# Performance work log

Measured on AMD Instinct MI355X. Metric: run time of the kernel, lower is better.

## Reference

```python
import jax, jax.numpy as jnp
import numpy as np

B, S = 128, 128
AH, VH, TH = 64, 64, 128  # audio/vision/text LSTM hidden sizes
FUSED = (AH + 1) * (VH + 1) * (TH + 1)  # 545025
PF = 128  # post_fusion_dim


def setup_inputs() -> dict:
    key = jax.random.key(0)
    ks = jax.random.split(key, 6)
    return {
        "audio_h": jax.random.normal(ks[0], (B, S, AH), jnp.float32),
        "vision_h": jax.random.normal(ks[1], (B, S, VH), jnp.float32),
        "text_h": jax.random.normal(ks[2], (B, S, TH), jnp.float32),
        "W1": jax.random.normal(ks[3], (PF, FUSED), jnp.float32) * 0.001,
        "b1": jnp.zeros((PF,), jnp.float32),
        "W2": jax.random.normal(ks[4], (PF, PF), jnp.float32) * 0.05,
        "b2": jnp.zeros((PF,), jnp.float32),
        "W3": jax.random.normal(ks[5], (1, PF), jnp.float32) * 0.05,
        "b3": jnp.zeros((1,), jnp.float32),
    }


def reference(audio_h, vision_h, text_h, W1, b1, W2, b2, W3, b3):
    b, s = audio_h.shape[0], audio_h.shape[1]
    ones = jnp.ones((b, s, 1), audio_h.dtype)
    a = jnp.concatenate([ones, audio_h], axis=2)   # [B,S,AH+1]
    v = jnp.concatenate([ones, vision_h], axis=2)  # [B,S,VH+1]
    t = jnp.concatenate([ones, text_h], axis=2)    # [B,S,TH+1]
    # sum_t outer(a_t, v_t, t_t): one fused contraction over the time axis
    fusion = jnp.einsum('bsa,bsv,bsw->bavw', a, v, t)  # [B,AH+1,VH+1,TH+1]
    fusion = fusion.reshape(b, -1)                      # matches torch view order (a,v,t)
    # T2FN low-rank regularizer scale
    tmp = jnp.sqrt(jnp.asarray(AH * VH * TH / max(AH, VH, TH), jnp.float32))
    # post-fusion MLP (dropout p=0 -> identity)
    y1 = jax.nn.relu(fusion @ W1.T + b1)
    y2 = jax.nn.relu(y1 @ W2.T + b2)
    out = y2 @ W3.T + b3  # [B,1]
    out = jax.nn.sigmoid(out) * 6.0 - 3.0  # output_range=6, output_shift=-3
    norm = jnp.linalg.norm(fusion, axis=1)  # [B]
    reg_loss = jnp.mean(tmp * norm)
    return (out, reg_loss)
```

## Files before the change

### kernel.cpp

```cpp
#include <hip/hip_runtime.h>
#include <math.h>

#define BB 128
#define SS 128
#define AE 65
#define VE 65
#define TE 129
#define PFD 128
#define FUSED 545025UL
#define FUSEDI 545025
#define VSTRIDE 136
#define APLANE 8840
#define FPP 574976UL
#define FPPI 574976
#define KSP 512
#define NBLK 1123

typedef _Float16 half8 __attribute__((ext_vector_type(8)));
typedef float f32x16 __attribute__((ext_vector_type(16)));

__device__ __forceinline__ void gll4(const void* g, void* l) {
  __builtin_amdgcn_global_load_lds((const __attribute__((address_space(1))) void*)g,
                                   (__attribute__((address_space(3))) void*)l, 4, 0, 0);
}
__device__ __forceinline__ void gll16(const void* g, void* l) {
  __builtin_amdgcn_global_load_lds((const __attribute__((address_space(1))) void*)g,
                                   (__attribute__((address_space(3))) void*)l, 16, 0, 0);
}

__global__ __launch_bounds__(256) void k_zero(float* __restrict__ p, int n) {
  int i = blockIdx.x * 256 + threadIdx.x;
  if (i < n) p[i] = 0.f;
}

__global__ __launch_bounds__(256) void k_fpad(_Float16* __restrict__ Fh) {
  const int b = blockIdx.x;
  _Float16* base = Fh + (size_t)b * FPP;
  for (int i = threadIdx.x; i < 29575; i += 256) {
    const int a = i / 455, r = i - a * 455;
    const int v = r / 7, e = r - v * 7;
    base[a * APLANE + v * VSTRIDE + 129 + e] = (_Float16)0.f;
  }
  for (int i = threadIdx.x; i < 376; i += 256) base[574600 + i] = (_Float16)0.f;
}

__global__ __launch_bounds__(256) void k_core(
    const float* __restrict__ audio, const float* __restrict__ vision,
    const float* __restrict__ text, _Float16* __restrict__ Fh,
    float* __restrict__ normsq)
{
  const int b  = blockIdx.x;
  const int gy = blockIdx.y;
  const int gz = blockIdx.z;
  const int tid = threadIdx.x;
  const int wv = tid >> 6, ln = tid & 63;
  const int lr = ln & 31, hb = ln >> 5;

  __shared__ float    sVt[64][132];
  __shared__ float    sAc[8][132];
  __shared__ _Float16 sTh[64][136];
  __shared__ _Float16 sTl[64][136];

  {
    const float* vb = vision + (size_t)b * SS * 64;
#pragma unroll
    for (int r = 0; r < 32; ++r) {
      const int e = tid + 256 * r;
      sVt[e & 63][e >> 6] = vb[e];
    }
    const float* ab = audio + (size_t)b * SS * 64 + 8 * gy;
#pragma unroll
    for (int r = 0; r < 4; ++r) {
      const int e = tid + 256 * r;
      sAc[e & 7][e >> 3] = ab[(e >> 3) * 64 + (e & 7)];
    }
    const int wbase = 64 * gz;
    const float* tb = text + (size_t)b * SS * 128;
#pragma unroll
    for (int r = 0; r < 32; ++r) {
      const int e = tid + 256 * r;
      const int s = e >> 6, wl = e & 63;
      const int w = wbase + wl;
      const float val = (w == 0) ? 1.f : tb[s * 128 + w - 1];
      const _Float16 th = (_Float16)val;
      sTh[wl][s] = th;
      sTl[wl][s] = (_Float16)((val - (float)th) * 2048.f);
    }
  }
  __syncthreads();

  float ss = 0.f;
  for (int i = 0; i < 8; ++i) {
    const int u  = 8 * wv + i;
    const int rt = u >> 1, wt = u & 1;
    const int j  = rt >> 1, vh = rt & 1;
    const int v0m = 32 * vh;
    const int wl0 = 32 * wt;

    f32x16 acc = {}, accl = {};
#pragma unroll
    for (int ks = 0; ks < 8; ++ks) {
      const int s0 = 16 * ks + 8 * hb;
      const float4 x0 = *(const float4*)&sVt[v0m + lr][s0];
      const float4 x1 = *(const float4*)&sVt[v0m + lr][s0 + 4];
      const float4 a0 = *(const float4*)&sAc[j][s0];
      const float4 a1 = *(const float4*)&sAc[j][s0 + 4];
      const float pp[8] = {a0.x * x0.x, a0.y * x0.y, a0.z * x0.z, a0.w * x0.w,
                           a1.x * x1.x, a1.y * x1.y, a1.z * x1.z, a1.w * x1.w};
      half8 afh, afl;
#pragma unroll
      for (int e = 0; e < 8; ++e) {
        const _Float16 h = (_Float16)pp[e];
        afh[e] = h;
        afl[e] = (_Float16)((pp[e] - (float)h) * 2048.f);
      }
      const half8 bqh = *(const half8*)&sTh[wl0 + lr][s0];
      const half8 bql = *(const half8*)&sTl[wl0 + lr][s0];
      acc  = __builtin_amdgcn_mfma_f32_32x32x16_f16(afh, bqh, acc,  0, 0, 0);
      accl = __builtin_amdgcn_mfma_f32_32x32x16_f16(afl, bqh, accl, 0, 0, 0);
      accl = __builtin_amdgcn_mfma_f32_32x32x16_f16(afh, bql, accl, 0, 0, 0);
    }

    const int a = 1 + 8 * gy + j;
    _Float16* Fb = Fh + (size_t)b * FPP + (size_t)a * APLANE;
    const int wg = 64 * gz + wl0 + lr;
#pragma unroll
    for (int reg = 0; reg < 16; ++reg) {
      const int crow = (reg & 3) + 8 * (reg >> 2) + 4 * hb;
      const int v = 1 + 32 * vh + crow;
      const float f = acc[reg] + accl[reg] * (1.f / 2048.f);
      ss += f * f;
      Fb[(size_t)v * VSTRIDE + wg] = (_Float16)f;
    }
  }

#pragma unroll
  for (int off = 32; off > 0; off >>= 1) ss += __shfl_down(ss, off);
  if (ln == 0) atomicAdd(&normsq[b], ss);
}

__global__ __launch_bounds__(256) void k_pa(
    const float* __restrict__ vision, const float* __restrict__ text,
    _Float16* __restrict__ Fh, float* __restrict__ normsq)
{
  const int b = blockIdx.x;
  const int tid = threadIdx.x;
  const int tw = tid & 15, tv = tid >> 4;
  __shared__ float sv[32][80];
  __shared__ float st[32][144];
  float acc[5][9];
#pragma unroll
  for (int i = 0; i < 5; ++i)
#pragma unroll
    for (int j = 0; j < 9; ++j) acc[i][j] = 0.f;

  for (int c = 0; c < 4; ++c) {
    const int s0 = 32 * c;
    __syncthreads();
    const float* vbase = &vision[((size_t)(b * SS + s0)) * 64];
#pragma unroll
    for (int r = 0; r < 8; ++r) {
      const int e = tid + 256 * r;
      sv[e >> 6][(e & 63) + 1] = vbase[e];
    }
    const float* tbase = &text[((size_t)(b * SS + s0)) * 128];
#pragma unroll
    for (int r = 0; r < 16; ++r) {
      const int e = tid + 256 * r;
      st[e >> 7][(e & 127) + 1] = tbase[e];
    }
    if (tid < 32) { sv[tid][0] = 1.f; st[tid][0] = 1.f; }
    __syncthreads();
    for (int s = 0; s < 32; ++s) {
      float vr[5], tr[9];
#pragma unroll
      for (int i = 0; i < 5; ++i) {
        const int vx = tv + 16 * i;
        vr[i] = (vx < VE) ? sv[s][vx] : 0.f;
      }
#pragma unroll
      for (int j = 0; j < 9; ++j) {
        const int wx = tw + 16 * j;
        tr[j] = (wx < TE) ? st[s][wx] : 0.f;
      }
#pragma unroll
      for (int i = 0; i < 5; ++i)
#pragma unroll
        for (int j = 0; j < 9; ++j) acc[i][j] += vr[i] * tr[j];
    }
  }
  _Float16* Fb = Fh + (size_t)b * FPP;
  float ss = 0.f;
#pragma unroll
  for (int i = 0; i < 5; ++i) {
    const int v = tv + 16 * i;
    if (v < VE) {
#pragma unroll
      for (int j = 0; j < 9; ++j) {
        const int w = tw + 16 * j;
        if (w < TE) {
          const float m = acc[i][j];
          Fb[(size_t)v * VSTRIDE + w] = (_Float16)m;
          ss += m * m;
        }
      }
    }
  }
#pragma unroll
  for (int off = 32; off > 0; off >>= 1) ss += __shfl_down(ss, off);
  if ((tid & 63) == 0) atomicAdd(&normsq[b], ss);
}

__global__ __launch_bounds__(256) void k_pv(
    const float* __restrict__ audio, const float* __restrict__ text,
    _Float16* __restrict__ Fh, float* __restrict__ normsq)
{
  const int b = blockIdx.x;
  const int tid = threadIdx.x;
  const int tw = tid & 15, tv = tid >> 4;
  __shared__ float sa[32][64];
  __shared__ float st[32][144];
  float acc[4][9];
#pragma unroll
  for (int i = 0; i < 4; ++i)
#pragma unroll
    for (int j = 0; j < 9; ++j) acc[i][j] = 0.f;

  for (int c = 0; c < 4; ++c) {
    const int s0 = 32 * c;
    __syncthreads();
    const float* abase = &audio[((size_t)(b * SS + s0)) * 64];
#pragma unroll
    for (int r = 0; r < 8; ++r) {
      const int e = tid + 256 * r;
      sa[e >> 6][e & 63] = abase[e];
    }
    const float* tbase = &text[((size_t)(b * SS + s0)) * 128];
#pragma unroll
    for (int r = 0; r < 16; ++r) {
      const int e = tid + 256 * r;
      st[e >> 7][(e & 127) + 1] = tbase[e];
    }
    if (tid < 32) st[tid][0] = 1.f;
    __syncthreads();
    for (int s = 0; s < 32; ++s) {
      float ar[4], tr[9];
#pragma unroll
      for (int i = 0; i < 4; ++i) ar[i] = sa[s][tv + 16 * i];
#pragma unroll
      for (int j = 0; j < 9; ++j) {
        const int wx = tw + 16 * j;
        tr[j] = (wx < TE) ? st[s][wx] : 0.f;
      }
#pragma unroll
      for (int i = 0; i < 4; ++i)
#pragma unroll
        for (int j = 0; j < 9; ++j) acc[i][j] += ar[i] * tr[j];
    }
  }
  float ss = 0.f;
#pragma unroll
  for (int i = 0; i < 4; ++i) {
    const int a = 1 + tv + 16 * i;
    _Float16* Fb = Fh + (size_t)b * FPP + (size_t)a * APLANE;
#pragma unroll
    for (int j = 0; j < 9; ++j) {
      const int w = tw + 16 * j;
      if (w < TE) {
        const float m = acc[i][j];
        Fb[w] = (_Float16)m;
        ss += m * m;
      }
    }
  }
#pragma unroll
  for (int off = 32; off > 0; off >>= 1) ss += __shfl_down(ss, off);
  if ((tid & 63) == 0) atomicAdd(&normsq[b], ss);
}

__global__ __launch_bounds__(256) void k_wlast(
    const float* __restrict__ audio, const float* __restrict__ vision,
    const float* __restrict__ text, _Float16* __restrict__ Fh,
    float* __restrict__ Flast, float* __restrict__ normsq)
{
  const int b = blockIdx.x;
  const int tid = threadIdx.x;
  const int tw = tid & 15, tv = tid >> 4;
  __shared__ float sa[32][64];
  __shared__ float sv[32][64];
  __shared__ float swt[32];
  float acc[4][4];
#pragma unroll
  for (int i = 0; i < 4; ++i)
#pragma unroll
    for (int j = 0; j < 4; ++j) acc[i][j] = 0.f;

  for (int c = 0; c < 4; ++c) {
    const int s0 = 32 * c;
    __syncthreads();
    const float* abase = &audio[((size_t)(b * SS + s0)) * 64];
    const float* vbase = &vision[((size_t)(b * SS + s0)) * 64];
#pragma unroll
    for (int r = 0; r < 8; ++r) {
      const int e = tid + 256 * r;
      sa[e >> 6][e & 63] = abase[e];
      sv[e >> 6][e & 63] = vbase[e];
    }
    if (tid < 32) swt[tid] = text[((size_t)(b * SS + s0 + tid)) * 128 + 127];
    __syncthreads();
    for (int s = 0; s < 32; ++s) {
      const float t = swt[s];
      float ar[4], vr[4];
#pragma unroll
      for (int i = 0; i < 4; ++i) ar[i] = sa[s][tv + 16 * i] * t;
#pragma unroll
      for (int j = 0; j < 4; ++j) vr[j] = sv[s][tw + 16 * j];
#pragma unroll
      for (int i = 0; i < 4; ++i)
#pragma unroll
        for (int j = 0; j < 4; ++j) acc[i][j] += ar[i] * vr[j];
    }
  }
  float ss = 0.f;
#pragma unroll
  for (int i = 0; i < 4; ++i) {
    const int a = 1 + tv + 16 * i;
    _Float16* Fb = Fh + (size_t)b * FPP + (size_t)a * APLANE;
#pragma unroll
    for (int j = 0; j < 4; ++j) {
      const int v = 1 + tw + 16 * j;
      float m = acc[i][j];
      ss += m * m;
      if (a == 64 && v == 64) { Flast[b] = m; m = 0.f; }
      Fb[(size_t)v * VSTRIDE + 128] = (_Float16)m;
    }
  }
#pragma unroll
  for (int off = 32; off > 0; off >>= 1) ss += __shfl_down(ss, off);
  if ((tid & 63) == 0) atomicAdd(&normsq[b], ss);
}

__global__ __launch_bounds__(256) void k_gemm(
    const float* __restrict__ W1, const _Float16* __restrict__ Fh,
    float* __restrict__ parts)
{
  __shared__ float    sA[2][4096];
  __shared__ _Float16 sB[2][4096];

  const int tid = threadIdx.x;
  const int wv = tid >> 6, ln = tid & 63;
  const int lb = ln & 31, hb = ln >> 5;
  const int p  = (wv << 5) + lb;
  const int kw = ln & 31;
  const int kp0 = blockIdx.x * KSP;

  int wtr[4], kot[4];
#pragma unroll
  for (int j = 0; j < 4; ++j) {
    const int slog = (kw >> 2) ^ ((2 * j + hb) & 7);
    const int kp = kp0 + (slog << 2) + (kw & 3);
    const int a = kp / APLANE;
    const int rem = kp - a * APLANE;
    const int vv = rem / VSTRIDE;
    wtr[j] = rem - vv * VSTRIDE;
    kot[j] = kp - a * 455 - vv * 7;
  }

  const int brow0 = (wv << 5) + (ln >> 2);
  const int slogB = (ln & 3) ^ ((ln >> 2) & 3);
  const _Float16* FhP0 = Fh + (size_t)brow0 * FPP + kp0 + (slogB << 3);
  const _Float16* FhP1 = FhP0 + (size_t)16 * FPP;

  const float* Wbase = W1 + (size_t)((wv << 5) + hb) * FUSED;

  f32x16 acc0 = {}, acc1 = {}, acc2 = {}, acc3 = {};

#define STAGE(BUF, KOFF)                                                        \
  {                                                                             \
    _Pragma("unroll")                                                           \
    for (int n = 0; n < 16; ++n) {                                              \
      const int kx = kot[n & 3];                                                \
      const int koc = (kx > 545024) ? 545024 : kx;                              \
      gll4(Wbase + (size_t)(2 * n) * FUSED + koc,                               \
           (char*)&sA[BUF][0] + (((wv << 5) + 2 * n) << 7));                    \
    }                                                                           \
    gll16(FhP0 + (KOFF), (char*)&sB[BUF][0] + ((wv << 5) << 6));                \
    gll16(FhP1 + (KOFF), (char*)&sB[BUF][0] + (((wv << 5) + 16) << 6));         \
    _Pragma("unroll")                                                           \
    for (int j = 0; j < 4; ++j) {                                               \
      wtr[j] += 32;                                                             \
      if (wtr[j] >= VSTRIDE) { wtr[j] -= VSTRIDE; kot[j] += 25; }               \
      else kot[j] += 32;                                                        \
    }                                                                           \
  }

  STAGE(0, 0)
  int buf = 0;
  for (int t = 0; t < 16; ++t) {
    __syncthreads();
    if (t + 1 < 16) STAGE(buf ^ 1, (t + 1) * 32)
    const float* sAb = &sA[buf][0];
    const _Float16* sBb = &sB[buf][0];
#pragma unroll
    for (int ks = 0; ks < 2; ++ks) {
      const int s0 = (ks << 2) + (hb << 1);
      const float4 x0 = *(const float4*)((const char*)sAb + (p << 7) + (((s0)     ^ (p & 7)) << 4));
      const float4 x1 = *(const float4*)((const char*)sAb + (p << 7) + (((s0 + 1) ^ (p & 7)) << 4));
      half8 af;
      af[0] = (_Float16)x0.x; af[1] = (_Float16)x0.y;
      af[2] = (_Float16)x0.z; af[3] = (_Float16)x0.w;
      af[4] = (_Float16)x1.x; af[5] = (_Float16)x1.y;
      af[6] = (_Float16)x1.z; af[7] = (_Float16)x1.w;
      const char* bbase = (const char*)sBb + (lb << 6) +
                          (((((ks << 1) + hb) ^ (lb & 3))) << 4);
      const half8 b0 = *(const half8*)(bbase);
      const half8 b1 = *(const half8*)(bbase + 2048);
      const half8 b2 = *(const half8*)(bbase + 4096);
      const half8 b3 = *(const half8*)(bbase + 6144);
      acc0 = __builtin_amdgcn_mfma_f32_32x32x16_f16(af, b0, acc0, 0, 0, 0);
      acc1 = __builtin_amdgcn_mfma_f32_32x32x16_f16(af, b1, acc1, 0, 0, 0);
      acc2 = __builtin_amdgcn_mfma_f32_32x32x16_f16(af, b2, acc2, 0, 0, 0);
      acc3 = __builtin_amdgcn_mfma_f32_32x32x16_f16(af, b3, acc3, 0, 0, 0);
    }
    buf ^= 1;
  }
#undef STAGE

  f32x16* o = (f32x16*)(parts + ((size_t)blockIdx.x * 256 + tid) * 64);
  o[0] = acc0; o[1] = acc1; o[2] = acc2; o[3] = acc3;
}

__global__ __launch_bounds__(256) void k_red(const float* __restrict__ parts,
                                             float* __restrict__ y1pre)
{
  const int tid = threadIdx.x;
  const int T = blockIdx.x * 4 + (tid >> 6);
  const int R = tid & 63;
  float s = 0.f;
  for (int sl = blockIdx.y; sl < NBLK; sl += 16)
    s += parts[(size_t)sl * 16384 + T * 64 + R];
  const int wv2 = T >> 6, hb2 = (T >> 5) & 1, lb2 = T & 31;
  const int q = R >> 4, rg = R & 15;
  const int b = q * 32 + lb2;
  const int pp = wv2 * 32 + (rg & 3) + 8 * (rg >> 2) + 4 * hb2;
  atomicAdd(&y1pre[b * PFD + pp], s);
}

__global__ __launch_bounds__(128) void k_final(
    const float* __restrict__ y1pre, const float* __restrict__ b1,
    const float* __restrict__ W2, const float* __restrict__ b2,
    const float* __restrict__ W3, const float* __restrict__ b3,
    const float* __restrict__ W1, const float* __restrict__ Flast,
    float* __restrict__ out)
{
  const int b = blockIdx.x, p = threadIdx.x;
  __shared__ float y1[PFD];
  __shared__ float red[PFD];
  const float extra = W1[(size_t)p * FUSED + (FUSED - 1)] * Flast[b];
  y1[p] = fmaxf(y1pre[(size_t)b * PFD + p] + extra + b1[p], 0.f);
  __syncthreads();
  float s = b2[p];
  for (int k = 0; k < PFD; ++k) s += y1[k] * W2[p * PFD + k];
  const float y2 = fmaxf(s, 0.f);
  red[p] = y2 * W3[p];
  __syncthreads();
  for (int off = 64; off > 0; off >>= 1) {
    if (p < off) red[p] += red[p + off];
    __syncthreads();
  }
  if (p == 0) {
    const float x = red[0] + b3[0];
    out[b] = 6.f / (1.f + expf(-x)) - 3.f;
  }
}

__global__ __launch_bounds__(128) void k_reg(const float* __restrict__ normsq,
                                             float* __restrict__ out)
{
  const int t = threadIdx.x;
  __shared__ float red[BB];
  red[t] = sqrtf(normsq[t]);
  __syncthreads();
  for (int off = 64; off > 0; off >>= 1) {
    if (t < off) red[t] += red[t + off];
    __syncthreads();
  }
  if (t == 0) out[BB] = 64.f * red[0] / (float)BB;
}

extern "C" void kernel_launch(void* const* d_in, const int* in_sizes, int n_in,
                              void* d_out, int out_size, void* d_ws, size_t ws_size,
                              hipStream_t stream) {
  const float* audio  = (const float*)d_in[0];
  const float* vision = (const float*)d_in[1];
  const float* text   = (const float*)d_in[2];
  const float* W1     = (const float*)d_in[3];
  const float* b1     = (const float*)d_in[4];
  const float* W2     = (const float*)d_in[5];
  const float* b2     = (const float*)d_in[6];
  const float* W3     = (const float*)d_in[7];
  const float* b3     = (const float*)d_in[8];
  float* out = (float*)d_out;

  float* y1pre  = (float*)d_ws;
  float* normsq = y1pre + BB * PFD;
  float* Flast  = normsq + BB;
  _Float16* Fh  = (_Float16*)((char*)d_ws + 131072);
  float* parts  = (float*)((char*)d_ws + 147324928);

  k_zero<<<65, 256, 0, stream>>>(y1pre, BB * PFD + 2 * BB);
  k_fpad<<<BB, 256, 0, stream>>>(Fh);

  k_core<<<dim3(BB, 8, 2), 256, 0, stream>>>(audio, vision, text, Fh, normsq);
  k_pa<<<BB, 256, 0, stream>>>(vision, text, Fh, normsq);
  k_pv<<<BB, 256, 0, stream>>>(audio, text, Fh, normsq);
  k_wlast<<<BB, 256, 0, stream>>>(audio, vision, text, Fh, Flast, normsq);

  k_gemm<<<NBLK, 256, 0, stream>>>(W1, Fh, parts);
  k_red<<<dim3(64, 16), 256, 0, stream>>>(parts, y1pre);

  k_final<<<BB, PFD, 0, stream>>>(y1pre, b1, W2, b2, W3, b3, W1, Flast, out);
  k_reg<<<1, BB, 0, stream>>>(normsq, out);
}
```

Baseline: 375.4 us.

## Load W1 via registers with 16-byte loads and convert to fp16 before LDS

```diff
diff --git a/kernel.cpp b/kernel.cpp
--- a/kernel.cpp
+++ b/kernel.cpp
@@ -19,10 +19,6 @@
 typedef _Float16 half8 __attribute__((ext_vector_type(8)));
 typedef float f32x16 __attribute__((ext_vector_type(16)));
 
-__device__ __forceinline__ void gll4(const void* g, void* l) {
-  __builtin_amdgcn_global_load_lds((const __attribute__((address_space(1))) void*)g,
-                                   (__attribute__((address_space(3))) void*)l, 4, 0, 0);
-}
 __device__ __forceinline__ void gll16(const void* g, void* l) {
   __builtin_amdgcn_global_load_lds((const __attribute__((address_space(1))) void*)g,
                                    (__attribute__((address_space(3))) void*)l, 16, 0, 0);
@@ -344,21 +340,23 @@
     const float* __restrict__ W1, const _Float16* __restrict__ Fh,
     float* __restrict__ parts)
 {
-  __shared__ float    sA[2][4096];
+  __shared__ _Float16 sA[2][4096];
   __shared__ _Float16 sB[2][4096];
 
   const int tid = threadIdx.x;
   const int wv = tid >> 6, ln = tid & 63;
   const int lb = ln & 31, hb = ln >> 5;
   const int p  = (wv << 5) + lb;
-  const int kw = ln & 31;
   const int kp0 = blockIdx.x * KSP;
 
+  const int arow = (wv << 5) + (ln >> 1);
+  const int kh = ln & 1;
+  const float* wrow = W1 + (size_t)arow * FUSED;
+
   int wtr[4], kot[4];
 #pragma unroll
   for (int j = 0; j < 4; ++j) {
-    const int slog = (kw >> 2) ^ ((2 * j + hb) & 7);
-    const int kp = kp0 + (slog << 2) + (kw & 3);
+    const int kp = kp0 + (kh << 4) + (j << 2);
     const int a = kp / APLANE;
     const int rem = kp - a * APLANE;
     const int vv = rem / VSTRIDE;
@@ -371,48 +369,69 @@
   const _Float16* FhP0 = Fh + (size_t)brow0 * FPP + kp0 + (slogB << 3);
   const _Float16* FhP1 = FhP0 + (size_t)16 * FPP;
 
-  const float* Wbase = W1 + (size_t)((wv << 5) + hb) * FUSED;
-
   f32x16 acc0 = {}, acc1 = {}, acc2 = {}, acc3 = {};
-
-#define STAGE(BUF, KOFF)                                                        \
-  {                                                                             \
-    _Pragma("unroll")                                                           \
-    for (int n = 0; n < 16; ++n) {                                              \
-      const int kx = kot[n & 3];                                                \
-      const int koc = (kx > 545024) ? 545024 : kx;                              \
-      gll4(Wbase + (size_t)(2 * n) * FUSED + koc,                               \
-           (char*)&sA[BUF][0] + (((wv << 5) + 2 * n) << 7));                    \
-    }                                                                           \
-    gll16(FhP0 + (KOFF), (char*)&sB[BUF][0] + ((wv << 5) << 6));                \
-    gll16(FhP1 + (KOFF), (char*)&sB[BUF][0] + (((wv << 5) + 16) << 6));         \
-    _Pragma("unroll")                                                           \
-    for (int j = 0; j < 4; ++j) {                                               \
-      wtr[j] += 32;                                                             \
-      if (wtr[j] >= VSTRIDE) { wtr[j] -= VSTRIDE; kot[j] += 25; }               \
-      else kot[j] += 32;                                                        \
-    }                                                                           \
-  }
-
-  STAGE(0, 0)
+  float4 xa[4];
+
+#define LOADA                                                              \
+  {                                                                        \
+    const int kc0 = (kot[0] <= 545021) ? kot[0] : 545021;                  \
+    const int kc1 = (kot[1] <= 545021) ? kot[1] : 545021;                  \
+    const int kc2 = (kot[2] <= 545021) ? kot[2] : 545021;                  \
+    const int kc3 = (kot[3] <= 545021) ? kot[3] : 545021;                  \
+    __builtin_memcpy(&xa[0], wrow + kc0, 16);                              \
+    __builtin_memcpy(&xa[1], wrow + kc1, 16);                              \
+    __builtin_memcpy(&xa[2], wrow + kc2, 16);                              \
+    __builtin_memcpy(&xa[3], wrow + kc3, 16);                              \
+    _Pragma("unroll")                                                      \
+    for (int j = 0; j < 4; ++j) {                                          \
+      wtr[j] += 32;                                                        \
+      if (wtr[j] >= VSTRIDE) { wtr[j] -= VSTRIDE; kot[j] += 25; }          \
+      else kot[j] += 32;                                                   \
+    }                                                                      \
+  }
+
+#define WRITEA(BUF)                                                       \
+  {                                                                       \
+    half8 h0, h1;                                                         \
+    h0[0] = (_Float16)xa[0].x; h0[1] = (_Float16)xa[0].y;                 \
+    h0[2] = (_Float16)xa[0].z; h0[3] = (_Float16)xa[0].w;                 \
+    h0[4] = (_Float16)xa[1].x; h0[5] = (_Float16)xa[1].y;                 \
+    h0[6] = (_Float16)xa[1].z; h0[7] = (_Float16)xa[1].w;                 \
+    h1[0] = (_Float16)xa[2].x; h1[1] = (_Float16)xa[2].y;                 \
+    h1[2] = (_Float16)xa[2].z; h1[3] = (_Float16)xa[2].w;                 \
+    h1[4] = (_Float16)xa[3].x; h1[5] = (_Float16)xa[3].y;                 \
+    h1[6] = (_Float16)xa[3].z; h1[7] = (_Float16)xa[3].w;                 \
+    const int sl0 = kh << 1;                                              \
+    *(half8*)((char*)&sA[BUF][0] + (arow << 6) +                          \
+              (((sl0)     ^ (arow & 3)) << 4)) = h0;                      \
+    *(half8*)((char*)&sA[BUF][0] + (arow << 6) +                          \
+              (((sl0 + 1) ^ (arow & 3)) << 4)) = h1;                      \
+  }
+
+#define STAGEB(BUF, KOFF)                                                 \
+  {                                                                       \
+    gll16(FhP0 + (KOFF), (char*)&sB[BUF][0] + ((wv << 5) << 6));          \
+    gll16(FhP1 + (KOFF), (char*)&sB[BUF][0] + (((wv << 5) + 16) << 6));   \
+  }
+
+  LOADA
+  STAGEB(0, 0)
+  WRITEA(0)
+  __syncthreads();
+
   int buf = 0;
   for (int t = 0; t < 16; ++t) {
-    __syncthreads();
-    if (t + 1 < 16) STAGE(buf ^ 1, (t + 1) * 32)
-    const float* sAb = &sA[buf][0];
+    if (t + 1 < 16) {
+      LOADA
+      STAGEB(buf ^ 1, (t + 1) * 32)
+    }
+    const _Float16* sAb = &sA[buf][0];
     const _Float16* sBb = &sB[buf][0];
 #pragma unroll
     for (int ks = 0; ks < 2; ++ks) {
-      const int s0 = (ks << 2) + (hb << 1);
-      const float4 x0 = *(const float4*)((const char*)sAb + (p << 7) + (((s0)     ^ (p & 7)) << 4));
-      const float4 x1 = *(const float4*)((const char*)sAb + (p << 7) + (((s0 + 1) ^ (p & 7)) << 4));
-      half8 af;
-      af[0] = (_Float16)x0.x; af[1] = (_Float16)x0.y;
-      af[2] = (_Float16)x0.z; af[3] = (_Float16)x0.w;
-      af[4] = (_Float16)x1.x; af[5] = (_Float16)x1.y;
-      af[6] = (_Float16)x1.z; af[7] = (_Float16)x1.w;
-      const char* bbase = (const char*)sBb + (lb << 6) +
-                          (((((ks << 1) + hb) ^ (lb & 3))) << 4);
+      const int sl = (ks << 1) + hb;
+      const half8 af = *(const half8*)((const char*)sAb + (p << 6) + ((sl ^ (p & 3)) << 4));
+      const char* bbase = (const char*)sBb + (lb << 6) + ((sl ^ (lb & 3)) << 4);
       const half8 b0 = *(const half8*)(bbase);
       const half8 b1 = *(const half8*)(bbase + 2048);
       const half8 b2 = *(const half8*)(bbase + 4096);
@@ -422,9 +441,13 @@
       acc2 = __builtin_amdgcn_mfma_f32_32x32x16_f16(af, b2, acc2, 0, 0, 0);
       acc3 = __builtin_amdgcn_mfma_f32_32x32x16_f16(af, b3, acc3, 0, 0, 0);
     }
+    if (t + 1 < 16) WRITEA(buf ^ 1)
+    __syncthreads();
     buf ^= 1;
   }
-#undef STAGE
+#undef LOADA
+#undef WRITEA
+#undef STAGEB
 
   f32x16* o = (f32x16*)(parts + ((size_t)blockIdx.x * 256 + tid) * 64);
   o[0] = acc0; o[1] = acc1; o[2] = acc2; o[3] = acc3;
```

Measured after the change: 393.7 us. 4.9% more time.
